# Performance work log

Hardware: AMD Instinct MI355X
Metric: run time of the kernel (lower is better)

The kernel has to match this reference:

```python
import jax, jax.numpy as jnp
import numpy as np

EPS = 1e-08
N_READS = 4
CELL_WIDTH = 64


def setup_inputs() -> dict:
    key = jax.random.key(0)
    ks = jax.random.split(key, 6)
    B, N, W, R = 8, 2048, CELL_WIDTH, N_READS
    memory = jax.random.normal(ks[0], (B, N, W), dtype=jnp.float32)
    controls = jax.random.normal(ks[1], (B, R * W + R + R * 3), dtype=jnp.float32)
    ww = jax.random.uniform(ks[2], (B, N), dtype=jnp.float32)
    write_weights = ww / ww.sum(-1, keepdims=True)  # simplex, as a DNC write head yields
    prev_links = jax.random.uniform(ks[3], (B, N, N), dtype=jnp.float32)
    prev_precedence = jax.random.uniform(ks[4], (B, N), dtype=jnp.float32)
    rw = jax.random.uniform(ks[5], (B, R, N), dtype=jnp.float32)
    prev_read_weights = rw / rw.sum(-1, keepdims=True)
    return {
        "memory": memory,
        "controls": controls,
        "write_weights": write_weights,
        "prev_links": prev_links,
        "prev_precedence": prev_precedence,
        "prev_read_weights": prev_read_weights,
    }


def reference(memory, controls, write_weights, prev_links, prev_precedence, prev_read_weights):
    B, N, W = memory.shape
    R = N_READS
    # --- split controls per self.shapes: [[R, W], R, [R, 3]] ---
    keys = controls[:, : R * W].reshape(B, R, W)
    betas = 1.0 + jax.nn.softplus(controls[:, R * W : R * W + R])  # [B, R]
    gates = jax.nn.softmax(controls[:, R * W + R :].reshape(B, R, 3), axis=-1)
    # --- content addressing: cosine similarity + softmax ---
    key_norm = jnp.linalg.norm(keys, axis=-1)    # [B, R]
    mem_norm = jnp.linalg.norm(memory, axis=-1)  # [B, N]
    dots = jnp.einsum("bnw,brw->brn", memory, keys)
    scores = dots / (key_norm[:, :, None] * mem_norm[:, None, :] + EPS)
    content_weights = jax.nn.softmax(scores * betas[:, :, None], axis=-1)  # [B, R, N]
    # --- temporal link matrix update ---
    wt_i = write_weights[:, :, None]          # [B, N, 1]
    wt_j = write_weights[:, None, :]          # [B, 1, N]
    pt_j = prev_precedence[:, None, :]        # [B, 1, N]
    diag_mask = 1.0 - jnp.eye(N, dtype=memory.dtype)
    links = ((1.0 - wt_i - wt_j) * prev_links + wt_i * pt_j) * diag_mask  # [B, N, N]
    # --- forward / backward weightings from prev read weights ---
    forward_weights = jnp.einsum("bij,brj->bri", links, prev_read_weights)
    backward_weights = jnp.einsum("bij,bri->brj", links, prev_read_weights)
    # --- mix via read modes ---
    read_weights = (
        gates[..., 0:1] * forward_weights
        + gates[..., 1:2] * backward_weights
        + gates[..., 2:3] * content_weights
    )  # [B, R, N]
    # --- read vector ---
    read_vector = jnp.einsum("bnw,brn->brw", memory, read_weights)  # [B, R, W]
    return read_vector
```

## Files before the change

### kernel.cpp

```cpp
#include <hip/hip_runtime.h>
#include <math.h>

#define BB 8
#define NN 2048
#define WWID 64
#define RNUM 4
#define CTRL 272
#define EPSF 1e-8f
#define TI 32
#define TILES 64
#define CQ 4

__device__ __forceinline__ float wred_sum(float v){
#pragma unroll
  for (int m=1;m<64;m<<=1) v += __shfl_xor(v,m);
  return v;
}
__device__ __forceinline__ float wred_max(float v){
#pragma unroll
  for (int m=1;m<64;m<<=1) v = fmaxf(v, __shfl_xor(v,m));
  return v;
}

__global__ __launch_bounds__(256) void k1_prep(
    const float* __restrict__ mem, const float* __restrict__ ctr,
    const float* __restrict__ ww, const float* __restrict__ prw,
    const float* __restrict__ L,
    float* __restrict__ scores, float* __restrict__ a_arr,
    float* __restrict__ Ldiag){
  int wid = threadIdx.x >> 6, lane = threadIdx.x & 63;
  int g = blockIdx.x * 4 + wid;
  int b = g >> 11, n = g & (NN-1);
  float m = mem[((size_t)(b*NN + n))*WWID + lane];
  const float* cb = ctr + b*CTRL;
  float k0 = cb[0*WWID+lane], k1 = cb[1*WWID+lane];
  float k2 = cb[2*WWID+lane], k3 = cb[3*WWID+lane];
  float s0 = m*m;
  float d0 = m*k0, d1 = m*k1, d2 = m*k2, d3 = m*k3;
  float q0 = k0*k0, q1 = k1*k1, q2 = k2*k2, q3 = k3*k3;
#pragma unroll
  for (int t=1;t<64;t<<=1){
    s0 += __shfl_xor(s0,t);
    d0 += __shfl_xor(d0,t); d1 += __shfl_xor(d1,t);
    d2 += __shfl_xor(d2,t); d3 += __shfl_xor(d3,t);
    q0 += __shfl_xor(q0,t); q1 += __shfl_xor(q1,t);
    q2 += __shfl_xor(q2,t); q3 += __shfl_xor(q3,t);
  }
  if (lane==0){
    float mn = sqrtf(s0);
    float be[4];
#pragma unroll
    for (int r=0;r<4;r++){
      float x = cb[RNUM*WWID + r];
      be[r] = 1.f + (x > 20.f ? x : log1pf(expf(x)));
    }
    scores[(b*RNUM+0)*NN+n] = d0*be[0]/(sqrtf(q0)*mn + EPSF);
    scores[(b*RNUM+1)*NN+n] = d1*be[1]/(sqrtf(q1)*mn + EPSF);
    scores[(b*RNUM+2)*NN+n] = d2*be[2]/(sqrtf(q2)*mn + EPSF);
    scores[(b*RNUM+3)*NN+n] = d3*be[3]/(sqrtf(q3)*mn + EPSF);
    Ldiag[b*NN+n] = L[((size_t)(b*NN+n))*NN + n];
  }
  if (lane < RNUM){
    int r = lane;
    a_arr[(b*RNUM+r)*NN+n] = (1.f - ww[b*NN+n]) * prw[(b*RNUM+r)*NN+n];
  }
}

__global__ __launch_bounds__(1024) void k2_head(
    const float* __restrict__ ctr, const float* __restrict__ scores,
    const float* __restrict__ ww, const float* __restrict__ prec,
    const float* __restrict__ prw, float* __restrict__ scal){
  __shared__ float redm[16], redS[16], redT[16], reds[16];
  int tid = threadIdx.x, wid = tid>>6, lane = tid&63;
  int b = blockIdx.x >> 2, r = blockIdx.x & 3;
  const float* sc = scores + (size_t)(b*RNUM+r)*NN;
  const float* pr = prw    + (size_t)(b*RNUM+r)*NN;
  float s0 = sc[tid], s1 = sc[tid+1024];
  float p0 = pr[tid], p1 = pr[tid+1024];
  float lmax = fmaxf(s0, s1);
  float lS = prec[b*NN+tid]*p0 + prec[b*NN+tid+1024]*p1;
  float lT = ww[b*NN+tid]*p0   + ww[b*NN+tid+1024]*p1;
  lmax = wred_max(lmax); lS = wred_sum(lS); lT = wred_sum(lT);
  if (lane==0){ redm[wid]=lmax; redS[wid]=lS; redT[wid]=lT; }
  __syncthreads();
  float mx=-1e30f, S=0.f, T=0.f;
#pragma unroll
  for (int i=0;i<16;i++){ mx=fmaxf(mx,redm[i]); S+=redS[i]; T+=redT[i]; }
  float ls = expf(s0-mx) + expf(s1-mx);
  ls = wred_sum(ls);
  if (lane==0) reds[wid]=ls;
  __syncthreads();
  float sum=0.f;
#pragma unroll
  for (int i=0;i<16;i++) sum += reds[i];
  if (tid==0){
    const float* cb = ctr + b*CTRL;
    float c0 = cb[RNUM*WWID + RNUM + r*3 + 0];
    float c1 = cb[RNUM*WWID + RNUM + r*3 + 1];
    float c2 = cb[RNUM*WWID + RNUM + r*3 + 2];
    float mg = fmaxf(c0, fmaxf(c1, c2));
    float e0 = expf(c0-mg), e1 = expf(c1-mg), e2 = expf(c2-mg);
    float inv3 = 1.f/(e0+e1+e2);
    float* s = &scal[(b*RNUM+r)*8];
    s[0]=e0*inv3; s[1]=e1*inv3; s[2]=e2*inv3;
    s[3]=S; s[4]=T; s[5]=mx; s[6]=1.f/sum;
  }
}

__global__ __launch_bounds__(256) void k3_links(
    const float* __restrict__ L, const float* __restrict__ ww,
    const float* __restrict__ prw, const float* __restrict__ a_arr,
    float* __restrict__ fwd_part, float* __restrict__ part){
  __shared__ float lrow[TI][16];
  __shared__ float lcol[4096];
  int tid = threadIdx.x, wid = tid>>6, lane = tid&63;
  int bid = blockIdx.x;
  int b   = bid >> 8;
  int rem = bid & 255;
  int tile = rem >> 2, cq = rem & 3;
  int i0 = tile*TI, jbase = cq*512;
  if (tid < TI){
    int i = i0 + tid;
    lrow[tid][0] = ww[b*NN + i];
#pragma unroll
    for (int r=0;r<RNUM;r++){
      lrow[tid][4+r] = a_arr[(b*RNUM+r)*NN + i];
      lrow[tid][8+r] = prw[(b*RNUM+r)*NN + i];
    }
  }
  __syncthreads();
  float accf[32];
#pragma unroll
  for (int k=0;k<32;k++) accf[k]=0.f;

  for (int c=0;c<2;c++){
    int j0 = jbase + c*256 + lane*4;
    float4 a4[4], p4[4];
#pragma unroll
    for (int r=0;r<4;r++){
      a4[r] = *reinterpret_cast<const float4*>(&a_arr[(b*RNUM+r)*NN + j0]);
      p4[r] = *reinterpret_cast<const float4*>(&prw[(b*RNUM+r)*NN + j0]);
    }
    float4 wwj = *reinterpret_cast<const float4*>(&ww[b*NN + j0]);
    float4 cacc[4];
#pragma unroll
    for (int r=0;r<4;r++){ cacc[r].x=0.f; cacc[r].y=0.f; cacc[r].z=0.f; cacc[r].w=0.f; }

#pragma unroll
    for (int rr=0; rr<8; rr++){
      int lr = wid*8 + rr;
      int i  = i0 + lr;
      float wwi = lrow[lr][0];
      float4 ai4 = *reinterpret_cast<const float4*>(&lrow[lr][4]);
      float4 pi4 = *reinterpret_cast<const float4*>(&lrow[lr][8]);
      float4 L4 = *reinterpret_cast<const float4*>(&L[((size_t)(b*NN + i))*NN + j0]);
#pragma unroll
      for (int r=0;r<4;r++){
        float4 ar = a4[r], pr = p4[r];
        float mx_ = fmaf(-wwi, pr.x, ar.x);
        float my_ = fmaf(-wwi, pr.y, ar.y);
        float mz_ = fmaf(-wwi, pr.z, ar.z);
        float mw_ = fmaf(-wwi, pr.w, ar.w);
        float s = accf[rr*4+r];
        s = fmaf(L4.x, mx_, s); s = fmaf(L4.y, my_, s);
        s = fmaf(L4.z, mz_, s); s = fmaf(L4.w, mw_, s);
        accf[rr*4+r] = s;
        float ai = (r==0)?ai4.x:((r==1)?ai4.y:((r==2)?ai4.z:ai4.w));
        float pi = (r==0)?pi4.x:((r==1)?pi4.y:((r==2)?pi4.z:pi4.w));
        float nx_ = fmaf(-wwj.x, pi, ai);
        float ny_ = fmaf(-wwj.y, pi, ai);
        float nz_ = fmaf(-wwj.z, pi, ai);
        float nw_ = fmaf(-wwj.w, pi, ai);
        cacc[r].x = fmaf(L4.x, nx_, cacc[r].x);
        cacc[r].y = fmaf(L4.y, ny_, cacc[r].y);
        cacc[r].z = fmaf(L4.z, nz_, cacc[r].z);
        cacc[r].w = fmaf(L4.w, nw_, cacc[r].w);
      }
    }
    __syncthreads();
#pragma unroll
    for (int r=0;r<4;r++)
      *reinterpret_cast<float4*>(&lcol[wid*1024 + r*256 + lane*4]) = cacc[r];
    __syncthreads();
    float4 v; v.x=0.f; v.y=0.f; v.z=0.f; v.w=0.f;
#pragma unroll
    for (int w=0;w<4;w++){
      float4 t = *reinterpret_cast<const float4*>(&lcol[w*1024 + wid*256 + lane*4]);
      v.x+=t.x; v.y+=t.y; v.z+=t.z; v.w+=t.w;
    }
    *reinterpret_cast<float4*>(
      &part[((size_t)((b*TILES+tile)*RNUM + wid))*NN + jbase + c*256 + lane*4]) = v;
  }

#pragma unroll
  for (int k=0;k<32;k++) accf[k] += __shfl_xor(accf[k], 32);
#pragma unroll
  for (int h=16; h>=1; h>>=1){
#pragma unroll
    for (int i=0;i<h;i++){
      float a = accf[i], bb = accf[i+h];
      bool up = (lane & h) != 0;
      float lo = up ? bb : a;
      float hi = up ? a : bb;
      accf[i] = lo + __shfl_xor(hi, h);
    }
  }
  if (lane < 32){
    int k = lane;
    fwd_part[((size_t)(b*CQ + cq)*RNUM + (k&3))*NN + i0 + wid*8 + (k>>2)] = accf[0];
  }
}

__global__ __launch_bounds__(256) void k4_combine(
    const float* __restrict__ part, const float* __restrict__ fwd_part,
    const float* __restrict__ scores, const float* __restrict__ scal,
    const float* __restrict__ ww, const float* __restrict__ prec,
    const float* __restrict__ prw, const float* __restrict__ Ldiag,
    float* __restrict__ rw){
  int b = blockIdx.x >> 5, rem = blockIdx.x & 31;
  int r = rem >> 3, nb = rem & 7;
  int n = nb*256 + threadIdx.x;
  const float* s = &scal[(b*RNUM+r)*8];
  float g0=s[0], g1=s[1], g2=s[2], S=s[3], T=s[4], mx=s[5], inv=s[6];
  const float* pp = part + ((size_t)(b*TILES)*RNUM + r)*NN + n;
  float b0=0.f,b1=0.f,b2=0.f,b3=0.f;
  for (int t=0;t<TILES;t+=4){
    b0 += pp[(size_t)(t+0)*RNUM*NN];
    b1 += pp[(size_t)(t+1)*RNUM*NN];
    b2 += pp[(size_t)(t+2)*RNUM*NN];
    b3 += pp[(size_t)(t+3)*RNUM*NN];
  }
  float bsum = (b0+b1)+(b2+b3);
  float fsum = 0.f;
#pragma unroll
  for (int cq=0;cq<CQ;cq++)
    fsum += fwd_part[((size_t)(b*CQ + cq)*RNUM + r)*NN + n];
  float wwn = ww[b*NN+n], pn = prec[b*NN+n], prn = prw[(b*RNUM+r)*NN+n];
  float Lnn = Ldiag[b*NN+n];
  float diag = (fmaf(-2.f*wwn, Lnn, Lnn) + wwn*pn) * prn;
  float fwd = fsum + wwn*S - diag;
  float bwd = bsum + pn*T - diag;
  float content = expf(scores[(b*RNUM+r)*NN+n] - mx) * inv;
  rw[(b*RNUM+r)*NN+n] = g0*fwd + g1*bwd + g2*content;
}

__global__ __launch_bounds__(256) void k5_read(
    const float* __restrict__ mem, const float* __restrict__ rw,
    float* __restrict__ out){
  __shared__ float rwl[256];
  int tid = threadIdx.x;
  int b = blockIdx.x >> 5, ch = blockIdx.x & 31;
  int n0 = ch*64;
  int r = tid >> 6, nn = tid & 63;
  rwl[tid] = rw[(b*RNUM+r)*NN + n0 + nn];
  __syncthreads();
  int wid = tid>>6, lane = tid&63;
  float acc = 0.f;
#pragma unroll 4
  for (int q=0; q<64; q++)
    acc = fmaf(mem[((size_t)(b*NN + n0 + q))*WWID + lane], rwl[wid*64+q], acc);
  atomicAdd(&out[(b*RNUM+wid)*WWID + lane], acc);
}

extern "C" void kernel_launch(void* const* d_in, const int* in_sizes, int n_in,
                              void* d_out, int out_size, void* d_ws, size_t ws_size,
                              hipStream_t stream){
  const float* mem  = (const float*)d_in[0];
  const float* ctr  = (const float*)d_in[1];
  const float* ww   = (const float*)d_in[2];
  const float* L    = (const float*)d_in[3];
  const float* prec = (const float*)d_in[4];
  const float* prw  = (const float*)d_in[5];
  float* out = (float*)d_out;
  float* w = (float*)d_ws;

  float* scores   = w;
  float* a_arr    = scores + BB*RNUM*NN;
  float* Ldiag    = a_arr + BB*RNUM*NN;
  float* scal     = Ldiag + BB*NN;
  float* fwd_part = scal + 256;
  float* rw       = fwd_part + BB*CQ*RNUM*NN;
  float* part     = rw + BB*RNUM*NN;

  hipMemsetAsync(out, 0, (size_t)BB*RNUM*WWID*sizeof(float), stream);
  k1_prep<<<BB*NN/4, 256, 0, stream>>>(mem, ctr, ww, prw, L, scores, a_arr, Ldiag);
  k2_head<<<BB*RNUM, 1024, 0, stream>>>(ctr, scores, ww, prec, prw, scal);
  k3_links<<<BB*TILES*CQ, 256, 0, stream>>>(L, ww, prw, a_arr, fwd_part, part);
  k4_combine<<<BB*RNUM*8, 256, 0, stream>>>(part, fwd_part, scores, scal, ww, prec, prw, Ldiag, rw);
  k5_read<<<BB*32, 256, 0, stream>>>(mem, rw, out);
}
```

Baseline: 252.7 us.

## Compute link-matrix products with bf16 MFMA and transposed LDS reads

The link-matrix kernel now converts L tiles to bf16 and runs both the forward and backward products on MFMA 16x16x32 instructions. The backward (transposed) product reads the tile through ds_read_b64_tr_b16. Read weights are prepacked into a bf16 operand matrix and the (1-w) factor is folded in afterwards. The softmax max-subtraction is dropped and the final read kernel uses a per-(b,r) reduction instead of atomics. This trades precision (bf16 L and weights, and possible exp overflow without the max shift) for removing the FP32 FMA bound on the 128 MB L stream.

New measurement: 267.3 us. +5.8%, slower.

```diff
diff --git a/kernel.cpp b/kernel.cpp
--- a/kernel.cpp
+++ b/kernel.cpp
@@ -1,4 +1,5 @@
 #include <hip/hip_runtime.h>
+#include <hip/hip_bf16.h>
 #include <math.h>
 
 #define BB 8
@@ -7,31 +8,32 @@
 #define RNUM 4
 #define CTRL 272
 #define EPSF 1e-8f
-#define TI 32
-#define TILES 64
-#define CQ 4
+
+typedef __attribute__((ext_vector_type(8))) short short8v;
+typedef __attribute__((ext_vector_type(4))) float f32x4;
+typedef __attribute__((ext_vector_type(2))) int int2v;
 
 __device__ __forceinline__ float wred_sum(float v){
 #pragma unroll
   for (int m=1;m<64;m<<=1) v += __shfl_xor(v,m);
   return v;
 }
-__device__ __forceinline__ float wred_max(float v){
-#pragma unroll
-  for (int m=1;m<64;m<<=1) v = fmaxf(v, __shfl_xor(v,m));
-  return v;
+
+__device__ __forceinline__ short bf16c(float f){
+  __hip_bfloat16 h = __float2bfloat16(f);
+  return *reinterpret_cast<short*>(&h);
 }
 
 __global__ __launch_bounds__(256) void k1_prep(
     const float* __restrict__ mem, const float* __restrict__ ctr,
     const float* __restrict__ ww, const float* __restrict__ prw,
     const float* __restrict__ L,
-    float* __restrict__ scores, float* __restrict__ a_arr,
-    float* __restrict__ Ldiag){
-  int wid = threadIdx.x >> 6, lane = threadIdx.x & 63;
-  int g = blockIdx.x * 4 + wid;
+    float* __restrict__ scores, float* __restrict__ Ldiag,
+    unsigned short* __restrict__ Xt){
+  int tid = threadIdx.x, wid = tid>>6, lane = tid&63;
+  int g = blockIdx.x*4 + wid;
   int b = g >> 11, n = g & (NN-1);
-  float m = mem[((size_t)(b*NN + n))*WWID + lane];
+  float m = mem[((size_t)g)*WWID + lane];
   const float* cb = ctr + b*CTRL;
   float k0 = cb[0*WWID+lane], k1 = cb[1*WWID+lane];
   float k2 = cb[2*WWID+lane], k3 = cb[3*WWID+lane];
@@ -58,11 +60,16 @@
     scores[(b*RNUM+1)*NN+n] = d1*be[1]/(sqrtf(q1)*mn + EPSF);
     scores[(b*RNUM+2)*NN+n] = d2*be[2]/(sqrtf(q2)*mn + EPSF);
     scores[(b*RNUM+3)*NN+n] = d3*be[3]/(sqrtf(q3)*mn + EPSF);
-    Ldiag[b*NN+n] = L[((size_t)(b*NN+n))*NN + n];
-  }
-  if (lane < RNUM){
-    int r = lane;
-    a_arr[(b*RNUM+r)*NN+n] = (1.f - ww[b*NN+n]) * prw[(b*RNUM+r)*NN+n];
+    Ldiag[b*NN+n] = L[((size_t)g)*NN + n];
+  }
+  if (tid < 64){
+    int v = tid & 15, n4 = tid >> 4;
+    int g2 = blockIdx.x*4 + n4;
+    int b2 = g2>>11, n2 = g2&(NN-1);
+    float val = 0.f;
+    if (v < 4)      val = prw[((size_t)b2*RNUM+v)*NN + n2];
+    else if (v < 8) val = ww[(size_t)b2*NN+n2] * prw[((size_t)b2*RNUM+(v-4))*NN + n2];
+    Xt[((size_t)b2*16 + v)*NN + n2] = (unsigned short)bf16c(val);
   }
 }
 
@@ -70,30 +77,23 @@
     const float* __restrict__ ctr, const float* __restrict__ scores,
     const float* __restrict__ ww, const float* __restrict__ prec,
     const float* __restrict__ prw, float* __restrict__ scal){
-  __shared__ float redm[16], redS[16], redT[16], reds[16];
-  int tid = threadIdx.x, wid = tid>>6, lane = tid&63;
-  int b = blockIdx.x >> 2, r = blockIdx.x & 3;
+  __shared__ float redS[16], redT[16], redE[16];
+  int tid=threadIdx.x, wid=tid>>6, lane=tid&63;
+  int b = blockIdx.x>>2, r = blockIdx.x&3;
   const float* sc = scores + (size_t)(b*RNUM+r)*NN;
   const float* pr = prw    + (size_t)(b*RNUM+r)*NN;
-  float s0 = sc[tid], s1 = sc[tid+1024];
-  float p0 = pr[tid], p1 = pr[tid+1024];
-  float lmax = fmaxf(s0, s1);
+  float s0=sc[tid], s1=sc[tid+1024];
+  float p0=pr[tid], p1=pr[tid+1024];
+  float lE = expf(s0)+expf(s1);
   float lS = prec[b*NN+tid]*p0 + prec[b*NN+tid+1024]*p1;
   float lT = ww[b*NN+tid]*p0   + ww[b*NN+tid+1024]*p1;
-  lmax = wred_max(lmax); lS = wred_sum(lS); lT = wred_sum(lT);
-  if (lane==0){ redm[wid]=lmax; redS[wid]=lS; redT[wid]=lT; }
+  lE=wred_sum(lE); lS=wred_sum(lS); lT=wred_sum(lT);
+  if (lane==0){ redE[wid]=lE; redS[wid]=lS; redT[wid]=lT; }
   __syncthreads();
-  float mx=-1e30f, S=0.f, T=0.f;
-#pragma unroll
-  for (int i=0;i<16;i++){ mx=fmaxf(mx,redm[i]); S+=redS[i]; T+=redT[i]; }
-  float ls = expf(s0-mx) + expf(s1-mx);
-  ls = wred_sum(ls);
-  if (lane==0) reds[wid]=ls;
-  __syncthreads();
-  float sum=0.f;
-#pragma unroll
-  for (int i=0;i<16;i++) sum += reds[i];
   if (tid==0){
+    float S=0.f,T=0.f,E=0.f;
+#pragma unroll
+    for(int i=0;i<16;i++){ S+=redS[i]; T+=redT[i]; E+=redE[i]; }
     const float* cb = ctr + b*CTRL;
     float c0 = cb[RNUM*WWID + RNUM + r*3 + 0];
     float c1 = cb[RNUM*WWID + RNUM + r*3 + 1];
@@ -103,111 +103,79 @@
     float inv3 = 1.f/(e0+e1+e2);
     float* s = &scal[(b*RNUM+r)*8];
     s[0]=e0*inv3; s[1]=e1*inv3; s[2]=e2*inv3;
-    s[3]=S; s[4]=T; s[5]=mx; s[6]=1.f/sum;
+    s[3]=S; s[4]=T; s[5]=1.f/E;
   }
 }
 
 __global__ __launch_bounds__(256) void k3_links(
-    const float* __restrict__ L, const float* __restrict__ ww,
-    const float* __restrict__ prw, const float* __restrict__ a_arr,
+    const float* __restrict__ L, const unsigned short* __restrict__ Xt,
     float* __restrict__ fwd_part, float* __restrict__ part){
-  __shared__ float lrow[TI][16];
-  __shared__ float lcol[4096];
-  int tid = threadIdx.x, wid = tid>>6, lane = tid&63;
+  __shared__ __attribute__((aligned(16))) unsigned short tile[4096];
+  int tid = threadIdx.x, w = tid>>6, l = tid&63;
+  int lrow = l & 15, lgrp = l >> 4;
   int bid = blockIdx.x;
-  int b   = bid >> 8;
-  int rem = bid & 255;
-  int tile = rem >> 2, cq = rem & 3;
-  int i0 = tile*TI, jbase = cq*512;
-  if (tid < TI){
-    int i = i0 + tid;
-    lrow[tid][0] = ww[b*NN + i];
-#pragma unroll
-    for (int r=0;r<RNUM;r++){
-      lrow[tid][4+r] = a_arr[(b*RNUM+r)*NN + i];
-      lrow[tid][8+r] = prw[(b*RNUM+r)*NN + i];
+  int b = bid >> 7;
+  int rem = bid & 127;
+  int ib = rem >> 2, jq = rem & 3;
+  int i0 = ib*64, j0b = jq*512;
+
+  const unsigned short* xb = Xt + (size_t)b*16*NN;
+  short8v afc0 = *(const short8v*)&xb[(size_t)lrow*NN + i0 +      lgrp*8];
+  short8v afc1 = *(const short8v*)&xb[(size_t)lrow*NN + i0 + 32 + lgrp*8];
+
+  f32x4 accRow = {0.f,0.f,0.f,0.f};
+  int irel = w*16 + lrow;
+  int wbase = (irel>>2)*256 + (irel&3)*16;
+  unsigned lbase = (unsigned)(size_t)(&tile[0]) + (unsigned)(lgrp*1024 + w*128 + lrow*2);
+
+  for (int sc=0; sc<8; ++sc){
+    int j0 = j0b + sc*64;
+    const float* Lr = L + ((size_t)(b*NN + i0 + w*16 + lrow))*NN + j0 + lgrp*8;
+    f32x4 La0 = __builtin_nontemporal_load((const f32x4*)Lr);
+    f32x4 La1 = __builtin_nontemporal_load((const f32x4*)(Lr+4));
+    f32x4 Lb0 = __builtin_nontemporal_load((const f32x4*)(Lr+32));
+    f32x4 Lb1 = __builtin_nontemporal_load((const f32x4*)(Lr+36));
+    short8v a0, a1;
+#pragma unroll
+    for (int e=0;e<4;e++){ a0[e]=bf16c(La0[e]); a0[4+e]=bf16c(La1[e]); }
+#pragma unroll
+    for (int e=0;e<4;e++){ a1[e]=bf16c(Lb0[e]); a1[4+e]=bf16c(Lb1[e]); }
+
+    __syncthreads();
+    int jr0 = lgrp*8;
+    *(short8v*)&tile[wbase + (jr0>>4)*64 + (jr0&15)] = a0;
+    int jr1 = 32 + lgrp*8;
+    *(short8v*)&tile[wbase + (jr1>>4)*64 + (jr1&15)] = a1;
+    __syncthreads();
+
+    short8v b0 = *(const short8v*)&xb[(size_t)lrow*NN + j0 +      lgrp*8];
+    short8v b1 = *(const short8v*)&xb[(size_t)lrow*NN + j0 + 32 + lgrp*8];
+    accRow = __builtin_amdgcn_mfma_f32_16x16x32_bf16(a0, b0, accRow, 0,0,0);
+    accRow = __builtin_amdgcn_mfma_f32_16x16x32_bf16(a1, b1, accRow, 0,0,0);
+
+    int2v t00,t01,t10,t11;
+    asm volatile("ds_read_b64_tr_b16 %0, %1 offset:0"    : "=v"(t00) : "v"(lbase));
+    asm volatile("ds_read_b64_tr_b16 %0, %1 offset:512"  : "=v"(t01) : "v"(lbase));
+    asm volatile("ds_read_b64_tr_b16 %0, %1 offset:4096" : "=v"(t10) : "v"(lbase));
+    asm volatile("ds_read_b64_tr_b16 %0, %1 offset:4608" : "=v"(t11) : "v"(lbase));
+    asm volatile("s_waitcnt lgkmcnt(0)");
+    __builtin_amdgcn_sched_barrier(0);
+    union { int2v p[2]; short8v s; } bc0, bc1;
+    bc0.p[0]=t00; bc0.p[1]=t01;
+    bc1.p[0]=t10; bc1.p[1]=t11;
+    f32x4 colD = {0.f,0.f,0.f,0.f};
+    colD = __builtin_amdgcn_mfma_f32_16x16x32_bf16(afc0, bc0.s, colD, 0,0,0);
+    colD = __builtin_amdgcn_mfma_f32_16x16x32_bf16(afc1, bc1.s, colD, 0,0,0);
+    if (l < 32){
+      int jabs = j0 + w*16 + lrow;
+#pragma unroll
+      for (int q=0;q<4;q++)
+        part[((size_t)((b*32+ib)*8) + lgrp*4+q)*NN + jabs] = colD[q];
     }
   }
-  __syncthreads();
-  float accf[32];
-#pragma unroll
-  for (int k=0;k<32;k++) accf[k]=0.f;
-
-  for (int c=0;c<2;c++){
-    int j0 = jbase + c*256 + lane*4;
-    float4 a4[4], p4[4];
-#pragma unroll
-    for (int r=0;r<4;r++){
-      a4[r] = *reinterpret_cast<const float4*>(&a_arr[(b*RNUM+r)*NN + j0]);
-      p4[r] = *reinterpret_cast<const float4*>(&prw[(b*RNUM+r)*NN + j0]);
-    }
-    float4 wwj = *reinterpret_cast<const float4*>(&ww[b*NN + j0]);
-    float4 cacc[4];
-#pragma unroll
-    for (int r=0;r<4;r++){ cacc[r].x=0.f; cacc[r].y=0.f; cacc[r].z=0.f; cacc[r].w=0.f; }
-
-#pragma unroll
-    for (int rr=0; rr<8; rr++){
-      int lr = wid*8 + rr;
-      int i  = i0 + lr;
-      float wwi = lrow[lr][0];
-      float4 ai4 = *reinterpret_cast<const float4*>(&lrow[lr][4]);
-      float4 pi4 = *reinterpret_cast<const float4*>(&lrow[lr][8]);
-      float4 L4 = *reinterpret_cast<const float4*>(&L[((size_t)(b*NN + i))*NN + j0]);
-#pragma unroll
-      for (int r=0;r<4;r++){
-        float4 ar = a4[r], pr = p4[r];
-        float mx_ = fmaf(-wwi, pr.x, ar.x);
-        float my_ = fmaf(-wwi, pr.y, ar.y);
-        float mz_ = fmaf(-wwi, pr.z, ar.z);
-        float mw_ = fmaf(-wwi, pr.w, ar.w);
-        float s = accf[rr*4+r];
-        s = fmaf(L4.x, mx_, s); s = fmaf(L4.y, my_, s);
-        s = fmaf(L4.z, mz_, s); s = fmaf(L4.w, mw_, s);
-        accf[rr*4+r] = s;
-        float ai = (r==0)?ai4.x:((r==1)?ai4.y:((r==2)?ai4.z:ai4.w));
-        float pi = (r==0)?pi4.x:((r==1)?pi4.y:((r==2)?pi4.z:pi4.w));
-        float nx_ = fmaf(-wwj.x, pi, ai);
-        float ny_ = fmaf(-wwj.y, pi, ai);
-        float nz_ = fmaf(-wwj.z, pi, ai);
-        float nw_ = fmaf(-wwj.w, pi, ai);
-        cacc[r].x = fmaf(L4.x, nx_, cacc[r].x);
-        cacc[r].y = fmaf(L4.y, ny_, cacc[r].y);
-        cacc[r].z = fmaf(L4.z, nz_, cacc[r].z);
-        cacc[r].w = fmaf(L4.w, nw_, cacc[r].w);
-      }
-    }
-    __syncthreads();
-#pragma unroll
-    for (int r=0;r<4;r++)
-      *reinterpret_cast<float4*>(&lcol[wid*1024 + r*256 + lane*4]) = cacc[r];
-    __syncthreads();
-    float4 v; v.x=0.f; v.y=0.f; v.z=0.f; v.w=0.f;
-#pragma unroll
-    for (int w=0;w<4;w++){
-      float4 t = *reinterpret_cast<const float4*>(&lcol[w*1024 + wid*256 + lane*4]);
-      v.x+=t.x; v.y+=t.y; v.z+=t.z; v.w+=t.w;
-    }
-    *reinterpret_cast<float4*>(
-      &part[((size_t)((b*TILES+tile)*RNUM + wid))*NN + jbase + c*256 + lane*4]) = v;
-  }
-
-#pragma unroll
-  for (int k=0;k<32;k++) accf[k] += __shfl_xor(accf[k], 32);
-#pragma unroll
-  for (int h=16; h>=1; h>>=1){
-#pragma unroll
-    for (int i=0;i<h;i++){
-      float a = accf[i], bb = accf[i+h];
-      bool up = (lane & h) != 0;
-      float lo = up ? bb : a;
-      float hi = up ? a : bb;
-      accf[i] = lo + __shfl_xor(hi, h);
-    }
-  }
-  if (lane < 32){
-    int k = lane;
-    fwd_part[((size_t)(b*CQ + cq)*RNUM + (k&3))*NN + i0 + wid*8 + (k>>2)] = accf[0];
+  if (lrow < 8){
+    float* fp = fwd_part + ((size_t)((b*4+jq)*8) + lrow)*NN + i0 + w*16 + lgrp*4;
+    *(f32x4*)fp = accRow;
   }
 }
 
@@ -221,45 +189,49 @@
   int r = rem >> 3, nb = rem & 7;
   int n = nb*256 + threadIdx.x;
   const float* s = &scal[(b*RNUM+r)*8];
-  float g0=s[0], g1=s[1], g2=s[2], S=s[3], T=s[4], mx=s[5], inv=s[6];
-  const float* pp = part + ((size_t)(b*TILES)*RNUM + r)*NN + n;
-  float b0=0.f,b1=0.f,b2=0.f,b3=0.f;
-  for (int t=0;t<TILES;t+=4){
-    b0 += pp[(size_t)(t+0)*RNUM*NN];
-    b1 += pp[(size_t)(t+1)*RNUM*NN];
-    b2 += pp[(size_t)(t+2)*RNUM*NN];
-    b3 += pp[(size_t)(t+3)*RNUM*NN];
-  }
-  float bsum = (b0+b1)+(b2+b3);
-  float fsum = 0.f;
-#pragma unroll
-  for (int cq=0;cq<CQ;cq++)
-    fsum += fwd_part[((size_t)(b*CQ + cq)*RNUM + r)*NN + n];
+  float g0=s[0], g1=s[1], g2=s[2], S=s[3], T=s[4], inv=s[5];
+  float V=0.f, W=0.f;
+#pragma unroll
+  for (int jq=0;jq<4;jq++){
+    V += fwd_part[((size_t)((b*4+jq)*8) + r  )*NN + n];
+    W += fwd_part[((size_t)((b*4+jq)*8) + r+4)*NN + n];
+  }
+  float P=0.f, Q=0.f;
+#pragma unroll 8
+  for (int ib=0;ib<32;ib++){
+    P += part[((size_t)((b*32+ib)*8) + r  )*NN + n];
+    Q += part[((size_t)((b*32+ib)*8) + r+4)*NN + n];
+  }
   float wwn = ww[b*NN+n], pn = prec[b*NN+n], prn = prw[(b*RNUM+r)*NN+n];
   float Lnn = Ldiag[b*NN+n];
   float diag = (fmaf(-2.f*wwn, Lnn, Lnn) + wwn*pn) * prn;
-  float fwd = fsum + wwn*S - diag;
-  float bwd = bsum + pn*T - diag;
-  float content = expf(scores[(b*RNUM+r)*NN+n] - mx) * inv;
+  float fwd = fmaf(1.f-wwn, V, -W) + wwn*S - diag;
+  float bwd = fmaf(1.f-wwn, P, -Q) + pn*T - diag;
+  float content = expf(scores[(b*RNUM+r)*NN+n]) * inv;
   rw[(b*RNUM+r)*NN+n] = g0*fwd + g1*bwd + g2*content;
 }
 
 __global__ __launch_bounds__(256) void k5_read(
     const float* __restrict__ mem, const float* __restrict__ rw,
     float* __restrict__ out){
-  __shared__ float rwl[256];
-  int tid = threadIdx.x;
-  int b = blockIdx.x >> 5, ch = blockIdx.x & 31;
-  int n0 = ch*64;
-  int r = tid >> 6, nn = tid & 63;
-  rwl[tid] = rw[(b*RNUM+r)*NN + n0 + nn];
+  __shared__ float rl[NN];
+  __shared__ float red[4][WWID];
+  int tid=threadIdx.x, w=tid>>6, lane=tid&63;
+  int b = blockIdx.x>>2, r = blockIdx.x&3;
+  const float* rp = rw + (size_t)(b*RNUM+r)*NN;
+  { const f32x4* s4=(const f32x4*)rp; f32x4* d4=(f32x4*)rl;
+    d4[tid] = s4[tid]; d4[tid+256] = s4[tid+256]; }
   __syncthreads();
-  int wid = tid>>6, lane = tid&63;
   float acc = 0.f;
+  const float* mp = mem + (size_t)b*NN*WWID + (size_t)w*512*WWID + lane;
 #pragma unroll 4
-  for (int q=0; q<64; q++)
-    acc = fmaf(mem[((size_t)(b*NN + n0 + q))*WWID + lane], rwl[wid*64+q], acc);
-  atomicAdd(&out[(b*RNUM+wid)*WWID + lane], acc);
+  for (int k=0;k<512;k++)
+    acc = fmaf(mp[(size_t)k*WWID], rl[w*512+k], acc);
+  red[w][lane] = acc;
+  __syncthreads();
+  if (w==0)
+    out[((size_t)(b*RNUM+r))*WWID + lane] =
+      red[0][lane]+red[1][lane]+red[2][lane]+red[3][lane];
 }
 
 extern "C" void kernel_launch(void* const* d_in, const int* in_sizes, int n_in,
@@ -275,17 +247,16 @@
   float* w = (float*)d_ws;
 
   float* scores   = w;
-  float* a_arr    = scores + BB*RNUM*NN;
-  float* Ldiag    = a_arr + BB*RNUM*NN;
+  float* Ldiag    = scores + BB*RNUM*NN;
   float* scal     = Ldiag + BB*NN;
-  float* fwd_part = scal + 256;
-  float* rw       = fwd_part + BB*CQ*RNUM*NN;
-  float* part     = rw + BB*RNUM*NN;
-
-  hipMemsetAsync(out, 0, (size_t)BB*RNUM*WWID*sizeof(float), stream);
-  k1_prep<<<BB*NN/4, 256, 0, stream>>>(mem, ctr, ww, prw, L, scores, a_arr, Ldiag);
+  float* rw       = scal + 256;
+  float* fwd_part = rw + BB*RNUM*NN;
+  float* part     = fwd_part + BB*4*8*NN;
+  unsigned short* Xt = (unsigned short*)(part + (size_t)BB*32*8*NN);
+
+  k1_prep<<<BB*NN/4, 256, 0, stream>>>(mem, ctr, ww, prw, L, scores, Ldiag, Xt);
   k2_head<<<BB*RNUM, 1024, 0, stream>>>(ctr, scores, ww, prec, prw, scal);
-  k3_links<<<BB*TILES*CQ, 256, 0, stream>>>(L, ww, prw, a_arr, fwd_part, part);
+  k3_links<<<BB*32*4, 256, 0, stream>>>(L, Xt, fwd_part, part);
   k4_combine<<<BB*RNUM*8, 256, 0, stream>>>(part, fwd_part, scores, scal, ww, prec, prw, Ldiag, rw);
-  k5_read<<<BB*32, 256, 0, stream>>>(mem, rw, out);
-}
+  k5_read<<<BB*RNUM, 256, 0, stream>>>(mem, rw, out);
+}
```

## Fuse combine and read kernels, drop softmax max pass in head kernel

Applied to the files above, without the earlier changes.

Merges the read-weight combine kernel with the memory read kernel so read weights stay in shared memory instead of a global round trip, removing one launch. The head kernel skips the max reduction and second block sync, summing exp(score) directly. This removes a reduction pass, but exp without max subtraction can overflow when scores are large (large beta).

After: 250.0 us. About the same (-1.1%).

```diff
diff --git a/kernel.cpp b/kernel.cpp
--- a/kernel.cpp
+++ b/kernel.cpp
@@ -14,11 +14,6 @@
 __device__ __forceinline__ float wred_sum(float v){
 #pragma unroll
   for (int m=1;m<64;m<<=1) v += __shfl_xor(v,m);
-  return v;
-}
-__device__ __forceinline__ float wred_max(float v){
-#pragma unroll
-  for (int m=1;m<64;m<<=1) v = fmaxf(v, __shfl_xor(v,m));
   return v;
 }
 
@@ -70,30 +65,23 @@
     const float* __restrict__ ctr, const float* __restrict__ scores,
     const float* __restrict__ ww, const float* __restrict__ prec,
     const float* __restrict__ prw, float* __restrict__ scal){
-  __shared__ float redm[16], redS[16], redT[16], reds[16];
-  int tid = threadIdx.x, wid = tid>>6, lane = tid&63;
-  int b = blockIdx.x >> 2, r = blockIdx.x & 3;
+  __shared__ float redS[16], redT[16], redE[16];
+  int tid=threadIdx.x, wid=tid>>6, lane=tid&63;
+  int b = blockIdx.x>>2, r = blockIdx.x&3;
   const float* sc = scores + (size_t)(b*RNUM+r)*NN;
   const float* pr = prw    + (size_t)(b*RNUM+r)*NN;
-  float s0 = sc[tid], s1 = sc[tid+1024];
-  float p0 = pr[tid], p1 = pr[tid+1024];
-  float lmax = fmaxf(s0, s1);
+  float s0=sc[tid], s1=sc[tid+1024];
+  float p0=pr[tid], p1=pr[tid+1024];
+  float lE = expf(s0)+expf(s1);
   float lS = prec[b*NN+tid]*p0 + prec[b*NN+tid+1024]*p1;
   float lT = ww[b*NN+tid]*p0   + ww[b*NN+tid+1024]*p1;
-  lmax = wred_max(lmax); lS = wred_sum(lS); lT = wred_sum(lT);
-  if (lane==0){ redm[wid]=lmax; redS[wid]=lS; redT[wid]=lT; }
+  lE=wred_sum(lE); lS=wred_sum(lS); lT=wred_sum(lT);
+  if (lane==0){ redE[wid]=lE; redS[wid]=lS; redT[wid]=lT; }
   __syncthreads();
-  float mx=-1e30f, S=0.f, T=0.f;
-#pragma unroll
-  for (int i=0;i<16;i++){ mx=fmaxf(mx,redm[i]); S+=redS[i]; T+=redT[i]; }
-  float ls = expf(s0-mx) + expf(s1-mx);
-  ls = wred_sum(ls);
-  if (lane==0) reds[wid]=ls;
-  __syncthreads();
-  float sum=0.f;
-#pragma unroll
-  for (int i=0;i<16;i++) sum += reds[i];
   if (tid==0){
+    float S=0.f,T=0.f,E=0.f;
+#pragma unroll
+    for(int i=0;i<16;i++){ S+=redS[i]; T+=redT[i]; E+=redE[i]; }
     const float* cb = ctr + b*CTRL;
     float c0 = cb[RNUM*WWID + RNUM + r*3 + 0];
     float c1 = cb[RNUM*WWID + RNUM + r*3 + 1];
@@ -103,7 +91,7 @@
     float inv3 = 1.f/(e0+e1+e2);
     float* s = &scal[(b*RNUM+r)*8];
     s[0]=e0*inv3; s[1]=e1*inv3; s[2]=e2*inv3;
-    s[3]=S; s[4]=T; s[5]=mx; s[6]=1.f/sum;
+    s[3]=S; s[4]=T; s[5]=1.f/E;
   }
 }
 
@@ -211,17 +199,19 @@
   }
 }
 
-__global__ __launch_bounds__(256) void k4_combine(
+__global__ __launch_bounds__(256) void k45_combine_read(
     const float* __restrict__ part, const float* __restrict__ fwd_part,
     const float* __restrict__ scores, const float* __restrict__ scal,
     const float* __restrict__ ww, const float* __restrict__ prec,
     const float* __restrict__ prw, const float* __restrict__ Ldiag,
-    float* __restrict__ rw){
+    const float* __restrict__ mem, float* __restrict__ out){
+  __shared__ float rwl[256];
+  int tid = threadIdx.x;
   int b = blockIdx.x >> 5, rem = blockIdx.x & 31;
   int r = rem >> 3, nb = rem & 7;
-  int n = nb*256 + threadIdx.x;
+  int n = nb*256 + tid;
   const float* s = &scal[(b*RNUM+r)*8];
-  float g0=s[0], g1=s[1], g2=s[2], S=s[3], T=s[4], mx=s[5], inv=s[6];
+  float g0=s[0], g1=s[1], g2=s[2], S=s[3], T=s[4], inv=s[5];
   const float* pp = part + ((size_t)(b*TILES)*RNUM + r)*NN + n;
   float b0=0.f,b1=0.f,b2=0.f,b3=0.f;
   for (int t=0;t<TILES;t+=4){
@@ -240,26 +230,16 @@
   float diag = (fmaf(-2.f*wwn, Lnn, Lnn) + wwn*pn) * prn;
   float fwd = fsum + wwn*S - diag;
   float bwd = bsum + pn*T - diag;
-  float content = expf(scores[(b*RNUM+r)*NN+n] - mx) * inv;
-  rw[(b*RNUM+r)*NN+n] = g0*fwd + g1*bwd + g2*content;
-}
-
-__global__ __launch_bounds__(256) void k5_read(
-    const float* __restrict__ mem, const float* __restrict__ rw,
-    float* __restrict__ out){
-  __shared__ float rwl[256];
-  int tid = threadIdx.x;
-  int b = blockIdx.x >> 5, ch = blockIdx.x & 31;
-  int n0 = ch*64;
-  int r = tid >> 6, nn = tid & 63;
-  rwl[tid] = rw[(b*RNUM+r)*NN + n0 + nn];
+  float content = expf(scores[(b*RNUM+r)*NN+n]) * inv;
+  rwl[tid] = g0*fwd + g1*bwd + g2*content;
   __syncthreads();
-  int wid = tid>>6, lane = tid&63;
+  int w = tid>>6, lane = tid&63;
   float acc = 0.f;
+  const float* mp = mem + ((size_t)(b*NN + nb*256 + w*64))*WWID + lane;
 #pragma unroll 4
   for (int q=0; q<64; q++)
-    acc = fmaf(mem[((size_t)(b*NN + n0 + q))*WWID + lane], rwl[wid*64+q], acc);
-  atomicAdd(&out[(b*RNUM+wid)*WWID + lane], acc);
+    acc = fmaf(mp[(size_t)q*WWID], rwl[w*64+q], acc);
+  atomicAdd(&out[(b*RNUM+r)*WWID + lane], acc);
 }
 
 extern "C" void kernel_launch(void* const* d_in, const int* in_sizes, int n_in,
@@ -279,13 +259,12 @@
   float* Ldiag    = a_arr + BB*RNUM*NN;
   float* scal     = Ldiag + BB*NN;
   float* fwd_part = scal + 256;
-  float* rw       = fwd_part + BB*CQ*RNUM*NN;
-  float* part     = rw + BB*RNUM*NN;
+  float* part     = fwd_part + BB*CQ*RNUM*NN;
 
   hipMemsetAsync(out, 0, (size_t)BB*RNUM*WWID*sizeof(float), stream);
   k1_prep<<<BB*NN/4, 256, 0, stream>>>(mem, ctr, ww, prw, L, scores, a_arr, Ldiag);
   k2_head<<<BB*RNUM, 1024, 0, stream>>>(ctr, scores, ww, prec, prw, scal);
   k3_links<<<BB*TILES*CQ, 256, 0, stream>>>(L, ww, prw, a_arr, fwd_part, part);
-  k4_combine<<<BB*RNUM*8, 256, 0, stream>>>(part, fwd_part, scores, scal, ww, prec, prw, Ldiag, rw);
-  k5_read<<<BB*32, 256, 0, stream>>>(mem, rw, out);
-}
+  k45_combine_read<<<BB*RNUM*8, 256, 0, stream>>>(part, fwd_part, scores, scal,
+                                                  ww, prec, prw, Ldiag, mem, out);
+}
```
